# Kernel tuning notes

Measured on AMD Instinct MI355X. Metric: run time of the kernel, lower is better.

The kernel has to match this reference:

```python
import jax, jax.numpy as jnp
import numpy as np

E = 128          # embed_dim
CTX = 3 * E      # context_dim = 384 (graph_emb 2E + node_emb E)
B = 16
N = 1024
D_IN = 2 * CTX   # mamba inner dim (expand=2) = 768
D_ST = 16        # mamba_hidden_dim (SSM state size)
DT_R = CTX // 16 # dt_rank = 24
K = 4            # causal depthwise conv kernel
TAU = 1.0        # gs_tau
ITERS = 5        # gs_iters


def setup_inputs() -> dict:
    key = jax.random.key(0)
    ks = jax.random.split(key, 12)
    s = 0.02
    inp = {
        "graph_emb": jax.random.normal(ks[0], (B, 2 * E), jnp.float32),
        "node_emb": jax.random.normal(ks[1], (B, N, E), jnp.float32),
        "W_key": jax.random.normal(ks[2], (E, CTX), jnp.float32) * s,
        "rms_w": jnp.ones((CTX,), jnp.float32),
        "W_in": jax.random.normal(ks[3], (CTX, 2 * D_IN), jnp.float32) * s,
        "conv_w": jax.random.normal(ks[4], (D_IN, K), jnp.float32) * s,
        "conv_b": jnp.zeros((D_IN,), jnp.float32),
        "W_x": jax.random.normal(ks[5], (D_IN, DT_R + 2 * D_ST), jnp.float32) * s,
        "W_dt": jax.random.normal(ks[6], (DT_R, D_IN), jnp.float32) * s,
        "b_dt": jnp.full((D_IN,), -4.0, jnp.float32),  # softplus -> small positive dt
        "A_log": jnp.log(jnp.tile(jnp.arange(1, D_ST + 1, dtype=jnp.float32), (D_IN, 1))),
        "Dp": jnp.ones((D_IN,), jnp.float32),
        "W_out": jax.random.normal(ks[7], (D_IN, CTX), jnp.float32) * s,
        "gumbel_sink": jax.random.gumbel(ks[8], (B, N, N), jnp.float32),
        "gumbel_sample": jax.random.gumbel(ks[9], (B, N, N), jnp.float32),
    }
    return inp


def _mamba(x, rms_w, W_in, conv_w, conv_b, W_x, W_dt, b_dt, A_log, Dp, W_out):
    # x: (B, N, CTX) -> (B, N, CTX); RMSNorm -> S6 mixer -> residual
    h = x * jax.lax.rsqrt(jnp.mean(x * x, axis=-1, keepdims=True) + 1e-6) * rms_w
    u, z = jnp.split(h @ W_in, 2, axis=-1)              # each (B, N, D_IN)
    # causal depthwise conv over the sequence axis
    uc = jnp.transpose(u, (0, 2, 1))                    # (B, D_IN, N)
    uc = jax.lax.conv_general_dilated(
        uc, conv_w[:, None, :], (1,), [(K - 1, 0)],
        dimension_numbers=("NCH", "OIH", "NCH"), feature_group_count=D_IN)
    u = jax.nn.silu(jnp.transpose(uc, (0, 2, 1)) + conv_b)  # (B, N, D_IN)
    dbc = u @ W_x                                       # (B, N, DT_R + 2*D_ST)
    dt, Bm, Cm = jnp.split(dbc, [DT_R, DT_R + D_ST], axis=-1)
    delta = jax.nn.softplus(dt @ W_dt + b_dt)           # (B, N, D_IN)
    A = -jnp.exp(A_log)                                 # (D_IN, D_ST)

    def step(hst, t):
        u_t, d_t, B_t, C_t = t                          # (B,D_IN),(B,D_IN),(B,D_ST),(B,D_ST)
        dA = jnp.exp(d_t[:, :, None] * A)               # (B, D_IN, D_ST)
        hst = dA * hst + (d_t * u_t)[:, :, None] * B_t[:, None, :]
        y = jnp.sum(hst * C_t[:, None, :], axis=-1)     # (B, D_IN)
        return hst, y

    seq = (jnp.transpose(u, (1, 0, 2)), jnp.transpose(delta, (1, 0, 2)),
           jnp.transpose(Bm, (1, 0, 2)), jnp.transpose(Cm, (1, 0, 2)))
    h0 = jnp.zeros((x.shape[0], D_IN, D_ST), x.dtype)
    _, ys = jax.lax.scan(step, h0, seq)                 # ys: (N, B, D_IN)
    y = jnp.transpose(ys, (1, 0, 2)) + Dp * u
    y = y * jax.nn.silu(z)
    return x + y @ W_out


def reference(graph_emb, node_emb, W_key, rms_w, W_in, conv_w, conv_b, W_x,
              W_dt, b_dt, A_log, Dp, W_out, gumbel_sink, gumbel_sample):
    b, n, _ = node_emb.shape
    keys = node_emb @ W_key                             # (B, N, CTX)
    ctx = jnp.concatenate(
        [jnp.broadcast_to(graph_emb[:, None, :], (b, n, graph_emb.shape[-1])), node_emb], axis=-1)
    queries = _mamba(ctx, rms_w, W_in, conv_w, conv_b, W_x, W_dt, b_dt, A_log, Dp, W_out)
    logits = jnp.einsum("bic,bjc->bij", keys, queries)  # (B, N, N)
    # Gumbel-Sinkhorn in log domain; end on row (axis=2) normalization -> rows are log-probs
    la = (logits + gumbel_sink) / TAU
    for _ in range(ITERS):
        la = la - jax.nn.logsumexp(la, axis=1, keepdims=True)  # column scaling
        la = la - jax.nn.logsumexp(la, axis=2, keepdims=True)  # row scaling
    # sampled tour: per-step categorical via Gumbel-max over rows
    tours = jnp.argmax(la + gumbel_sample, axis=-1)     # (B, N) int
    log_probs = jnp.take_along_axis(la, tours[..., None], axis=2)[..., 0]  # (B, N)
    entropies = -jnp.sum(la * jnp.exp(la), axis=-1)     # (B, N)
    return tours, log_probs, entropies
```

## Files before the change

### kernel.cpp

```cpp
#include <hip/hip_runtime.h>
#include <math.h>

#define Bsz 16
#define Nn  1024
#define Ee  128
#define CTX 384
#define DIN 768
#define DST 16
#define DTR 24
#define ROWS (Bsz*Nn)

__global__ __launch_bounds__(128) void rms_k(
    const float* __restrict__ ge, const float* __restrict__ ne,
    float* __restrict__ rs)
{
    int row = blockIdx.x;
    int b = row >> 10;
    int tid = threadIdx.x;
    float ssq = 0.f;
    #pragma unroll
    for (int k = 0; k < 3; ++k) {
        int idx = tid + k * 128;
        float v = (idx < 256) ? ge[b * 256 + idx]
                              : ne[(long long)row * 128 + (idx - 256)];
        ssq += v * v;
    }
    __shared__ float sh[128];
    sh[tid] = ssq;
    __syncthreads();
    for (int w = 64; w > 0; w >>= 1) {
        if (tid < w) sh[tid] += sh[tid + w];
        __syncthreads();
    }
    if (tid == 0) rs[row] = rsqrtf(sh[0] * (1.f / 384.f) + 1e-6f);
}

__global__ __launch_bounds__(256) void zero_k(float* __restrict__ p, int n)
{
    int i = blockIdx.x * 256 + threadIdx.x;
    if (i < n) p[i] = 0.f;
}

template<int EPI, bool BT, int AMODE>
__global__ __launch_bounds__(256) void gemm_k(
    const float* __restrict__ A, int lda, long long aB,
    const float* __restrict__ Bm, int ldb, long long bB,
    float* __restrict__ C, int ldc, long long cB,
    int M, int N, int K,
    const float* __restrict__ ge, const float* __restrict__ ne,
    const float* __restrict__ rowS, const float* __restrict__ colS,
    const float* __restrict__ bias,
    const float* __restrict__ add, long long addB)
{
    __shared__ float As[16][68];
    __shared__ float Bs[16][68];
    int tid = threadIdx.x;
    int tx = tid & 15, ty = tid >> 4;
    int gn0 = blockIdx.x * 64;
    int rowBase = blockIdx.y * 64;
    int bz = blockIdx.z;
    const float* Ab = A + (long long)bz * aB + (long long)rowBase * lda;
    const float* Bb = Bm + (long long)bz * bB;
    float acc[4][4] = {};

    for (int k0 = 0; k0 < K; k0 += 16) {
        #pragma unroll
        for (int r = 0; r < 4; ++r) {
            int idx = tid + r * 256;
            int m = idx >> 4, kk = idx & 15;
            float v = 0.f;
            if (AMODE == 0) {
                if (k0 + kk < K) v = Ab[(long long)m * lda + k0 + kk];
            } else if (AMODE == 1) {
                int grow = rowBase + m;
                int col = k0 + kk;
                if (col < K) {
                    v = (col < 256) ? ge[(grow >> 10) * 256 + col]
                                    : ne[(long long)grow * 128 + (col - 256)];
                    v *= rowS[grow] * colS[col];
                }
            } else {
                int grow = rowBase + m;
                int col = k0 + kk;
                if (col < K) {
                    v = A[(long long)col * lda + grow];
                    if (AMODE == 3) {
                        float z = rowS[(long long)grow * 768 + col];
                        v *= z / (1.f + __expf(-z));
                    }
                }
            }
            As[kk][m] = v;
        }
        #pragma unroll
        for (int r = 0; r < 4; ++r) {
            int idx = tid + r * 256;
            if (!BT) {
                int n = idx & 63, kk = idx >> 6;
                float v = 0.f;
                if (k0 + kk < K && gn0 + n < N)
                    v = Bb[(long long)(k0 + kk) * ldb + gn0 + n];
                Bs[kk][n] = v;
            } else {
                int kk = idx & 15, n = idx >> 4;
                float v = 0.f;
                if (k0 + kk < K && gn0 + n < N)
                    v = Bb[(long long)(gn0 + n) * ldb + k0 + kk];
                Bs[kk][n] = v;
            }
        }
        __syncthreads();
        #pragma unroll
        for (int kk = 0; kk < 16; ++kk) {
            float4 a4 = *(const float4*)&As[kk][ty * 4];
            float4 b4 = *(const float4*)&Bs[kk][tx * 4];
            float av[4] = {a4.x, a4.y, a4.z, a4.w};
            float bv[4] = {b4.x, b4.y, b4.z, b4.w};
            #pragma unroll
            for (int i = 0; i < 4; ++i)
                #pragma unroll
                for (int j = 0; j < 4; ++j)
                    acc[i][j] = fmaf(av[i], bv[j], acc[i][j]);
        }
        __syncthreads();
    }

    #pragma unroll
    for (int i = 0; i < 4; ++i) {
        int gm = rowBase + ty * 4 + i;
        #pragma unroll
        for (int j = 0; j < 4; ++j) {
            int gn = gn0 + tx * 4 + j;
            if (gn >= N) continue;
            float v = acc[i][j];
            if (EPI == 1) {
                float x = v + bias[gn];
                v = fmaxf(x, 0.f) + log1pf(expf(-fabsf(x)));
            } else if (EPI == 3) {
                v += add[(long long)bz * addB + (long long)gm * (long long)N + gn];
            } else if (EPI == 4) {
                v += (gn < 256) ? ge[(gm >> 10) * 256 + gn]
                                : ne[(long long)gm * 128 + (gn - 256)];
            } else if (EPI == 5) {
                float x = v + bias[gm];
                v = fmaxf(x, 0.f) + log1pf(expf(-fabsf(x)));
            }
            C[(long long)bz * cB + (long long)gm * ldc + gn] = v;
        }
    }
}

__global__ __launch_bounds__(256) void conv_t_k(
    const float* __restrict__ uB, const float* __restrict__ cw,
    const float* __restrict__ cb, float* __restrict__ uT)
{
    __shared__ float tile[67][33];
    int b = blockIdx.z, d0 = blockIdx.y * 32, n0 = blockIdx.x * 64;
    int tid = threadIdx.x;
    for (int i = tid; i < 67 * 32; i += 256) {
        int r = i >> 5, c = i & 31;
        int n = n0 - 3 + r;
        tile[r][c] = (n >= 0) ? uB[((long long)(b * 1024 + n)) * 768 + d0 + c] : 0.f;
    }
    __syncthreads();
    int nl = tid & 63;
    int dh = (tid >> 6) * 8;
    #pragma unroll
    for (int dl = 0; dl < 8; ++dl) {
        int d = dh + dl;
        const float* w = cw + (d0 + d) * 4;
        float acc = cb[d0 + d];
        acc = fmaf(tile[nl][d],     w[0], acc);
        acc = fmaf(tile[nl + 1][d], w[1], acc);
        acc = fmaf(tile[nl + 2][d], w[2], acc);
        acc = fmaf(tile[nl + 3][d], w[3], acc);
        float sv = acc / (1.f + __expf(-acc));
        uT[(long long)(d0 + d) * 16384 + b * 1024 + n0 + nl] = sv;
    }
}

__global__ __launch_bounds__(256) void pack_bc_k(
    const float* __restrict__ dbc, float* __restrict__ TBC)
{
    int c = blockIdx.y;
    int gm = blockIdx.x * 256 + threadIdx.x;
    TBC[(long long)c * 16384 + gm] = dbc[(long long)gm * 56 + 24 + c];
}

__global__ __launch_bounds__(256) void scan2_k(
    const float* __restrict__ dT, float* uyT,
    const float* __restrict__ TBC, const float* __restrict__ A_log,
    const float* __restrict__ Dp)
{
    int tid = threadIdx.x;
    int s = tid & 15, dl = tid >> 4;
    int b = blockIdx.y;
    int d = blockIdx.x * 16 + dl;
    float a = -__expf(A_log[d * 16 + s]);
    float dp = Dp[d];
    long long base = (long long)b * 1024;
    const float* dR = dT + (long long)d * 16384 + base;
    const float* uR = uyT + (long long)d * 16384 + base;
    const float* BR = TBC + (long long)s * 16384 + base;
    const float* CR = TBC + (long long)(16 + s) * 16384 + base;
    float* yR = uyT + (long long)d * 16384 + base;

    float4 dv0 = *(const float4*)(dR);
    float4 dv1 = *(const float4*)(dR + 4);
    float4 uv0 = *(const float4*)(uR);
    float4 uv1 = *(const float4*)(uR + 4);
    float4 Bv0 = *(const float4*)(BR);
    float4 Bv1 = *(const float4*)(BR + 4);
    float4 Cv0 = *(const float4*)(CR);
    float4 Cv1 = *(const float4*)(CR + 4);
    float h = 0.f;

    for (int g = 0; g < 256; ++g) {
        int gp = (g + 2 < 256) ? (g + 2) * 4 : 255 * 4;
        float4 dv2 = *(const float4*)(dR + gp);
        float4 uv2 = *(const float4*)(uR + gp);
        float4 Bv2 = *(const float4*)(BR + gp);
        float4 Cv2 = *(const float4*)(CR + gp);

        float dv[4] = {dv0.x, dv0.y, dv0.z, dv0.w};
        float uv[4] = {uv0.x, uv0.y, uv0.z, uv0.w};
        float Bv[4] = {Bv0.x, Bv0.y, Bv0.z, Bv0.w};
        float Cv[4] = {Cv0.x, Cv0.y, Cv0.z, Cv0.w};
        float ya[4];
        #pragma unroll
        for (int j = 0; j < 4; ++j) {
            float dA = __expf(dv[j] * a);
            h = fmaf(dA, h, dv[j] * uv[j] * Bv[j]);
            float yp = h * Cv[j];
            yp += __shfl_down(yp, 8, 16);
            yp += __shfl_down(yp, 4, 16);
            yp += __shfl_down(yp, 2, 16);
            yp += __shfl_down(yp, 1, 16);
            ya[j] = yp + dp * uv[j];
        }
        if (s == 0) {
            *(float4*)(yR + g * 4) = make_float4(ya[0], ya[1], ya[2], ya[3]);
        }
        dv0 = dv1; dv1 = dv2;
        uv0 = uv1; uv1 = uv2;
        Bv0 = Bv1; Bv1 = Bv2;
        Cv0 = Cv1; Cv1 = Cv2;
    }
}

__global__ __launch_bounds__(256) void col_lse_part(
    const float* __restrict__ la0, const float* __restrict__ R,
    float2* __restrict__ cpart)
{
    int j = blockIdx.x * 256 + threadIdx.x;
    int ch = blockIdx.y;
    int b = blockIdx.z;
    const float* base = la0 + (long long)b * 1024 * 1024 + (long long)ch * 64 * 1024 + j;
    const float* Rb = R + b * 1024 + ch * 64;
    float m = -INFINITY, sum = 0.f;
    for (int i = 0; i < 64; ++i) {
        float x = base[(long long)i * 1024] - Rb[i];
        float nm = fmaxf(m, x);
        sum = sum * expf(m - nm) + expf(x - nm);
        m = nm;
    }
    cpart[(long long)(b * 16 + ch) * 1024 + j] = make_float2(m, sum);
}

__global__ __launch_bounds__(256) void col_comb_k(
    const float2* __restrict__ cpart, float* __restrict__ Cv)
{
    int idx = blockIdx.x * 256 + threadIdx.x;
    int b = idx >> 10, j = idx & 1023;
    float m = -INFINITY, sum = 0.f;
    #pragma unroll
    for (int ch = 0; ch < 16; ++ch) {
        float2 p = cpart[(long long)(b * 16 + ch) * 1024 + j];
        float nm = fmaxf(m, p.x);
        sum = sum * expf(m - nm) + p.y * expf(p.x - nm);
        m = nm;
    }
    Cv[idx] = m + logf(sum);
}

__global__ __launch_bounds__(256) void row_lse_k(
    const float* __restrict__ la0, const float* __restrict__ Cv,
    float* __restrict__ R)
{
    int r = blockIdx.x;
    int b = r >> 10;
    const float* row = la0 + (long long)r * 1024;
    const float* Cb = Cv + b * 1024;
    int tid = threadIdx.x;
    float m = -INFINITY, sum = 0.f;
    #pragma unroll
    for (int k = 0; k < 4; ++k) {
        int j = tid + k * 256;
        float x = row[j] - Cb[j];
        float nm = fmaxf(m, x);
        sum = sum * expf(m - nm) + expf(x - nm);
        m = nm;
    }
    __shared__ float sm[256], ss[256];
    sm[tid] = m; ss[tid] = sum;
    __syncthreads();
    for (int w = 128; w > 0; w >>= 1) {
        if (tid < w) {
            float m2 = sm[tid + w], s2 = ss[tid + w];
            float nm = fmaxf(sm[tid], m2);
            ss[tid] = ss[tid] * expf(sm[tid] - nm) + s2 * expf(m2 - nm);
            sm[tid] = nm;
        }
        __syncthreads();
    }
    if (tid == 0) R[r] = sm[0] + logf(ss[0]);
}

__global__ __launch_bounds__(256) void final_k(
    const float* __restrict__ la0, const float* __restrict__ R,
    const float* __restrict__ Cv, const float* __restrict__ gs,
    float* __restrict__ out)
{
    int r = blockIdx.x;
    int b = r >> 10;
    const float* row = la0 + (long long)r * 1024;
    const float* gr = gs + (long long)r * 1024;
    const float* Cb = Cv + b * 1024;
    float Rvv = R[r];
    int tid = threadIdx.x;
    float bestg = -INFINITY;
    int bestj = 1 << 30;
    float ent = 0.f;
    #pragma unroll
    for (int k = 0; k < 4; ++k) {
        int j = tid + k * 256;
        float la = row[j] - Rvv - Cb[j];
        ent += la * expf(la);
        float g = la + gr[j];
        if (g > bestg || (g == bestg && j < bestj)) { bestg = g; bestj = j; }
    }
    __shared__ float sg[256]; __shared__ int sj[256]; __shared__ float se[256];
    sg[tid] = bestg; sj[tid] = bestj; se[tid] = ent;
    __syncthreads();
    for (int w = 128; w > 0; w >>= 1) {
        if (tid < w) {
            se[tid] += se[tid + w];
            float g2 = sg[tid + w]; int j2 = sj[tid + w];
            if (g2 > sg[tid] || (g2 == sg[tid] && j2 < sj[tid])) {
                sg[tid] = g2; sj[tid] = j2;
            }
        }
        __syncthreads();
    }
    if (tid == 0) {
        int j = sj[0];
        out[r] = (float)j;
        out[16384 + r] = row[j] - Rvv - Cb[j];
        out[32768 + r] = -se[0];
    }
}

extern "C" void kernel_launch(void* const* d_in, const int* in_sizes, int n_in,
                              void* d_out, int out_size, void* d_ws, size_t ws_size,
                              hipStream_t stream)
{
    const float* graph_emb = (const float*)d_in[0];
    const float* node_emb  = (const float*)d_in[1];
    const float* W_key     = (const float*)d_in[2];
    const float* rms_w     = (const float*)d_in[3];
    const float* W_in      = (const float*)d_in[4];
    const float* conv_w    = (const float*)d_in[5];
    const float* conv_b    = (const float*)d_in[6];
    const float* W_x       = (const float*)d_in[7];
    const float* W_dt      = (const float*)d_in[8];
    const float* b_dt      = (const float*)d_in[9];
    const float* A_log     = (const float*)d_in[10];
    const float* Dp        = (const float*)d_in[11];
    const float* W_out     = (const float*)d_in[12];
    const float* g_sink    = (const float*)d_in[13];
    const float* g_samp    = (const float*)d_in[14];
    float* out = (float*)d_out;

    float* ws = (float*)d_ws;
    size_t o = 0;
    auto alloc = [&](size_t nf) { float* p = ws + o; o += nf; return p; };
    float* rs    = alloc(ROWS);
    float* dbc   = alloc((size_t)ROWS * 56);
    float* keys  = alloc((size_t)ROWS * 384);
    float* R1    = alloc((size_t)ROWS * 768);
    float* R2    = alloc((size_t)ROWS * 768);
    float* R3    = alloc((size_t)ROWS * 768);
    float* Rv    = alloc(ROWS);
    float* Cvec  = alloc(ROWS);
    float* cpart = alloc((size_t)16 * 16 * 1024 * 2);
    float* uB      = R1;
    float* deltaT  = R1;
    float* queries = R1;
    float* uT      = R2;
    float* zB      = R3;
    float* la0     = R2;
    float* TBC     = cpart;

    rms_k<<<dim3(ROWS), 128, 0, stream>>>(graph_emb, node_emb, rs);

    gemm_k<0, false, 0><<<dim3(6, 256, 1), 256, 0, stream>>>(
        node_emb, 128, 0, W_key, 384, 0, keys, 384, 0,
        ROWS, 384, 128, nullptr, nullptr, nullptr, nullptr, nullptr, nullptr, 0);

    gemm_k<0, false, 1><<<dim3(12, 256, 1), 256, 0, stream>>>(
        nullptr, 0, 0, W_in, 1536, 0, uB, 768, 0,
        ROWS, 768, 384, graph_emb, node_emb, rs, rms_w, nullptr, nullptr, 0);

    gemm_k<0, false, 1><<<dim3(12, 256, 1), 256, 0, stream>>>(
        nullptr, 0, 0, W_in + 768, 1536, 0, zB, 768, 0,
        ROWS, 768, 384, graph_emb, node_emb, rs, rms_w, nullptr, nullptr, 0);

    conv_t_k<<<dim3(16, 24, 16), 256, 0, stream>>>(uB, conv_w, conv_b, uT);

    gemm_k<0, false, 2><<<dim3(1, 256, 1), 256, 0, stream>>>(
        uT, 16384, 0, W_x, 56, 0, dbc, 56, 0,
        ROWS, 56, 768, nullptr, nullptr, nullptr, nullptr, nullptr, nullptr, 0);

    gemm_k<5, true, 2><<<dim3(256, 12, 1), 256, 0, stream>>>(
        W_dt, 768, 0, dbc, 56, 0, deltaT, 16384, 0,
        768, 16384, 24, nullptr, nullptr, nullptr, nullptr, b_dt, nullptr, 0);

    pack_bc_k<<<dim3(64, 32), 256, 0, stream>>>(dbc, TBC);

    scan2_k<<<dim3(48, 16), 256, 0, stream>>>(deltaT, uT, TBC, A_log, Dp);

    gemm_k<4, false, 3><<<dim3(6, 256, 1), 256, 0, stream>>>(
        uT, 16384, 0, W_out, 384, 0, queries, 384, 0,
        ROWS, 384, 768, graph_emb, node_emb, zB, nullptr, nullptr, nullptr, 0);

    gemm_k<3, true, 0><<<dim3(16, 16, 16), 256, 0, stream>>>(
        keys, 384, (long long)Nn * 384, queries, 384, (long long)Nn * 384,
        la0, 1024, (long long)Nn * Nn,
        1024, 1024, 384, nullptr, nullptr, nullptr, nullptr, nullptr,
        g_sink, (long long)Nn * Nn);

    zero_k<<<dim3(64), 256, 0, stream>>>(Rv, ROWS);
    for (int it = 0; it < 5; ++it) {
        col_lse_part<<<dim3(4, 16, 16), 256, 0, stream>>>(la0, Rv, (float2*)cpart);
        col_comb_k<<<dim3(64), 256, 0, stream>>>((const float2*)cpart, Cvec);
        row_lse_k<<<dim3(ROWS), 256, 0, stream>>>(la0, Cvec, Rv);
    }

    final_k<<<dim3(ROWS), 256, 0, stream>>>(la0, Rv, Cvec, g_samp, out);
}
```

Measured before the change: 1.787 ms.

## Use 128x128 register-blocked GEMM tiles and fuse SiLU gate into scan

Replaces the 64x64 tile / 4x4-per-thread GEMM with a 128x128 tile / 8x8-per-thread version. It uses vectorized float4 global loads and stores, and adds an optional transposed-output path. The z gate is now written transposed so the scan kernel can apply y*silu(z) directly, which removes the transposed gated loads from the out-projection GEMM. The aim is more arithmetic per shared-memory load and cheaper global traffic. The cost is higher register pressure, fewer blocks for the small GEMMs, and a transposed store pattern for z.

```diff
diff --git a/kernel.cpp b/kernel.cpp
--- a/kernel.cpp
+++ b/kernel.cpp
@@ -41,8 +41,8 @@
     if (i < n) p[i] = 0.f;
 }
 
-template<int EPI, bool BT, int AMODE>
-__global__ __launch_bounds__(256) void gemm_k(
+template<int EPI, bool BT, int AMODE, bool CT>
+__global__ __launch_bounds__(256) void gemm2_k(
     const float* __restrict__ A, int lda, long long aB,
     const float* __restrict__ Bm, int ldb, long long bB,
     float* __restrict__ C, int ldc, long long cB,
@@ -52,100 +52,153 @@
     const float* __restrict__ bias,
     const float* __restrict__ add, long long addB)
 {
-    __shared__ float As[16][68];
-    __shared__ float Bs[16][68];
-    int tid = threadIdx.x;
-    int tx = tid & 15, ty = tid >> 4;
-    int gn0 = blockIdx.x * 64;
-    int rowBase = blockIdx.y * 64;
+    __shared__ float As[16][132];
+    __shared__ float Bs[16][132];
+    int t = threadIdx.x;
+    int gn0 = blockIdx.x * 128;
+    int rowBase = blockIdx.y * 128;
     int bz = blockIdx.z;
-    const float* Ab = A + (long long)bz * aB + (long long)rowBase * lda;
+    const float* Abase = A + (long long)bz * aB;
     const float* Bb = Bm + (long long)bz * bB;
-    float acc[4][4] = {};
+    float acc[8][8] = {};
+
+    int cx4 = (t & 15) * 4;
+    int ry4 = (t >> 4) * 4;
 
     for (int k0 = 0; k0 < K; k0 += 16) {
-        #pragma unroll
-        for (int r = 0; r < 4; ++r) {
-            int idx = tid + r * 256;
-            int m = idx >> 4, kk = idx & 15;
-            float v = 0.f;
+        if (AMODE == 0 || AMODE == 1) {
+            int r = t >> 1;
+            int kq = (t & 1) * 8;
+            float av[8];
             if (AMODE == 0) {
-                if (k0 + kk < K) v = Ab[(long long)m * lda + k0 + kk];
-            } else if (AMODE == 1) {
-                int grow = rowBase + m;
-                int col = k0 + kk;
-                if (col < K) {
-                    v = (col < 256) ? ge[(grow >> 10) * 256 + col]
-                                    : ne[(long long)grow * 128 + (col - 256)];
-                    v *= rowS[grow] * colS[col];
-                }
+                const float* Ap = Abase + (long long)(rowBase + r) * lda + k0 + kq;
+                #pragma unroll
+                for (int j = 0; j < 8; ++j)
+                    av[j] = (k0 + kq + j < K) ? Ap[j] : 0.f;
             } else {
-                int grow = rowBase + m;
-                int col = k0 + kk;
-                if (col < K) {
-                    v = A[(long long)col * lda + grow];
-                    if (AMODE == 3) {
-                        float z = rowS[(long long)grow * 768 + col];
-                        v *= z / (1.f + __expf(-z));
+                int grow = rowBase + r;
+                float rsv = rowS[grow];
+                #pragma unroll
+                for (int j = 0; j < 8; ++j) {
+                    int col = k0 + kq + j;
+                    float v = 0.f;
+                    if (col < K) {
+                        v = (col < 256) ? ge[(grow >> 10) * 256 + col]
+                                        : ne[(long long)grow * 128 + (col - 256)];
+                        v *= rsv * colS[col];
                     }
+                    av[j] = v;
                 }
             }
-            As[kk][m] = v;
-        }
-        #pragma unroll
-        for (int r = 0; r < 4; ++r) {
-            int idx = tid + r * 256;
-            if (!BT) {
-                int n = idx & 63, kk = idx >> 6;
-                float v = 0.f;
-                if (k0 + kk < K && gn0 + n < N)
-                    v = Bb[(long long)(k0 + kk) * ldb + gn0 + n];
-                Bs[kk][n] = v;
-            } else {
-                int kk = idx & 15, n = idx >> 4;
-                float v = 0.f;
-                if (k0 + kk < K && gn0 + n < N)
-                    v = Bb[(long long)(gn0 + n) * ldb + k0 + kk];
-                Bs[kk][n] = v;
+            #pragma unroll
+            for (int j = 0; j < 8; ++j) As[kq + j][r] = av[j];
+        } else {
+            int kk = t >> 4;
+            int m0 = (t & 15) * 8;
+            const float* Ap = Abase + (long long)(k0 + kk) * lda + rowBase + m0;
+            float4 v0 = make_float4(0.f, 0.f, 0.f, 0.f), v1 = v0;
+            if (k0 + kk < K) {
+                v0 = *(const float4*)Ap;
+                v1 = *(const float4*)(Ap + 4);
             }
+            *(float4*)&As[kk][m0] = v0;
+            *(float4*)&As[kk][m0 + 4] = v1;
+        }
+        if (!BT) {
+            int kk = t >> 4;
+            int n0 = (t & 15) * 8;
+            const float* Bp = Bb + (long long)(k0 + kk) * ldb + gn0 + n0;
+            float4 v0 = make_float4(0.f, 0.f, 0.f, 0.f), v1 = v0;
+            if (k0 + kk < K) {
+                if (gn0 + n0 + 7 < N) {
+                    v0 = *(const float4*)Bp;
+                    v1 = *(const float4*)(Bp + 4);
+                } else {
+                    float tmp[8];
+                    #pragma unroll
+                    for (int j = 0; j < 8; ++j)
+                        tmp[j] = (gn0 + n0 + j < N) ? Bp[j] : 0.f;
+                    v0 = make_float4(tmp[0], tmp[1], tmp[2], tmp[3]);
+                    v1 = make_float4(tmp[4], tmp[5], tmp[6], tmp[7]);
+                }
+            }
+            *(float4*)&Bs[kk][n0] = v0;
+            *(float4*)&Bs[kk][n0 + 4] = v1;
+        } else {
+            int n = t >> 1;
+            int kq = (t & 1) * 8;
+            const float* Bp = Bb + (long long)(gn0 + n) * ldb + k0 + kq;
+            float bv[8];
+            bool nok = (gn0 + n < N);
+            #pragma unroll
+            for (int j = 0; j < 8; ++j)
+                bv[j] = (nok && k0 + kq + j < K) ? Bp[j] : 0.f;
+            #pragma unroll
+            for (int j = 0; j < 8; ++j) Bs[kq + j][n] = bv[j];
         }
         __syncthreads();
         #pragma unroll
         for (int kk = 0; kk < 16; ++kk) {
-            float4 a4 = *(const float4*)&As[kk][ty * 4];
-            float4 b4 = *(const float4*)&Bs[kk][tx * 4];
-            float av[4] = {a4.x, a4.y, a4.z, a4.w};
-            float bv[4] = {b4.x, b4.y, b4.z, b4.w};
+            float4 a0 = *(const float4*)&As[kk][ry4];
+            float4 a1 = *(const float4*)&As[kk][ry4 + 64];
+            float4 b0 = *(const float4*)&Bs[kk][cx4];
+            float4 b1 = *(const float4*)&Bs[kk][cx4 + 64];
+            float av[8] = {a0.x, a0.y, a0.z, a0.w, a1.x, a1.y, a1.z, a1.w};
+            float bv[8] = {b0.x, b0.y, b0.z, b0.w, b1.x, b1.y, b1.z, b1.w};
             #pragma unroll
-            for (int i = 0; i < 4; ++i)
+            for (int i = 0; i < 8; ++i)
                 #pragma unroll
-                for (int j = 0; j < 4; ++j)
+                for (int j = 0; j < 8; ++j)
                     acc[i][j] = fmaf(av[i], bv[j], acc[i][j]);
         }
         __syncthreads();
     }
 
-    #pragma unroll
-    for (int i = 0; i < 4; ++i) {
-        int gm = rowBase + ty * 4 + i;
+    if (CT) {
         #pragma unroll
-        for (int j = 0; j < 4; ++j) {
-            int gn = gn0 + tx * 4 + j;
-            if (gn >= N) continue;
-            float v = acc[i][j];
-            if (EPI == 1) {
-                float x = v + bias[gn];
-                v = fmaxf(x, 0.f) + log1pf(expf(-fabsf(x)));
-            } else if (EPI == 3) {
-                v += add[(long long)bz * addB + (long long)gm * (long long)N + gn];
-            } else if (EPI == 4) {
-                v += (gn < 256) ? ge[(gm >> 10) * 256 + gn]
-                                : ne[(long long)gm * 128 + (gn - 256)];
-            } else if (EPI == 5) {
-                float x = v + bias[gm];
-                v = fmaxf(x, 0.f) + log1pf(expf(-fabsf(x)));
+        for (int j = 0; j < 8; ++j) {
+            int gn = gn0 + (j >> 2) * 64 + cx4 + (j & 3);
+            #pragma unroll
+            for (int ih = 0; ih < 2; ++ih) {
+                int gmb = rowBase + ih * 64 + ry4;
+                float4 v = make_float4(acc[ih * 4 + 0][j], acc[ih * 4 + 1][j],
+                                       acc[ih * 4 + 2][j], acc[ih * 4 + 3][j]);
+                *(float4*)&C[(long long)gn * ldc + gmb] = v;
             }
-            C[(long long)bz * cB + (long long)gm * ldc + gn] = v;
+        }
+    } else {
+        float* Cb = C + (long long)bz * cB;
+        #pragma unroll
+        for (int i = 0; i < 8; ++i) {
+            int gm = rowBase + (i >> 2) * 64 + ry4 + (i & 3);
+            #pragma unroll
+            for (int jh = 0; jh < 2; ++jh) {
+                int gn = gn0 + jh * 64 + cx4;
+                float v[4];
+                #pragma unroll
+                for (int e = 0; e < 4; ++e) {
+                    float x = acc[i][jh * 4 + e];
+                    if (EPI == 3) {
+                        x += add[(long long)bz * addB + (long long)gm * (long long)N + gn + e];
+                    } else if (EPI == 4) {
+                        int c = gn + e;
+                        x += (c < 256) ? ge[(gm >> 10) * 256 + c]
+                                       : ne[(long long)gm * 128 + (c - 256)];
+                    } else if (EPI == 5) {
+                        float s = x + bias[gm];
+                        x = fmaxf(s, 0.f) + log1pf(expf(-fabsf(s)));
+                    }
+                    v[e] = x;
+                }
+                if (gn + 3 < N) {
+                    *(float4*)&Cb[(long long)gm * ldc + gn] =
+                        make_float4(v[0], v[1], v[2], v[3]);
+                } else {
+                    #pragma unroll
+                    for (int e = 0; e < 4; ++e)
+                        if (gn + e < N) Cb[(long long)gm * ldc + gn + e] = v[e];
+                }
+            }
         }
     }
 }
@@ -187,8 +240,8 @@
     TBC[(long long)c * 16384 + gm] = dbc[(long long)gm * 56 + 24 + c];
 }
 
-__global__ __launch_bounds__(256) void scan2_k(
-    const float* __restrict__ dT, float* uyT,
+__global__ __launch_bounds__(256) void scan3_k(
+    const float* __restrict__ dT, float* uyT, const float* __restrict__ zT,
     const float* __restrict__ TBC, const float* __restrict__ A_log,
     const float* __restrict__ Dp)
 {
@@ -201,6 +254,7 @@
     long long base = (long long)b * 1024;
     const float* dR = dT + (long long)d * 16384 + base;
     const float* uR = uyT + (long long)d * 16384 + base;
+    const float* zR = zT + (long long)d * 16384 + base;
     const float* BR = TBC + (long long)s * 16384 + base;
     const float* CR = TBC + (long long)(16 + s) * 16384 + base;
     float* yR = uyT + (long long)d * 16384 + base;
@@ -209,6 +263,8 @@
     float4 dv1 = *(const float4*)(dR + 4);
     float4 uv0 = *(const float4*)(uR);
     float4 uv1 = *(const float4*)(uR + 4);
+    float4 zv0 = *(const float4*)(zR);
+    float4 zv1 = *(const float4*)(zR + 4);
     float4 Bv0 = *(const float4*)(BR);
     float4 Bv1 = *(const float4*)(BR + 4);
     float4 Cv0 = *(const float4*)(CR);
@@ -219,11 +275,13 @@
         int gp = (g + 2 < 256) ? (g + 2) * 4 : 255 * 4;
         float4 dv2 = *(const float4*)(dR + gp);
         float4 uv2 = *(const float4*)(uR + gp);
+        float4 zv2 = *(const float4*)(zR + gp);
         float4 Bv2 = *(const float4*)(BR + gp);
         float4 Cv2 = *(const float4*)(CR + gp);
 
         float dv[4] = {dv0.x, dv0.y, dv0.z, dv0.w};
         float uv[4] = {uv0.x, uv0.y, uv0.z, uv0.w};
+        float zv[4] = {zv0.x, zv0.y, zv0.z, zv0.w};
         float Bv[4] = {Bv0.x, Bv0.y, Bv0.z, Bv0.w};
         float Cv[4] = {Cv0.x, Cv0.y, Cv0.z, Cv0.w};
         float ya[4];
@@ -236,13 +294,15 @@
             yp += __shfl_down(yp, 4, 16);
             yp += __shfl_down(yp, 2, 16);
             yp += __shfl_down(yp, 1, 16);
-            ya[j] = yp + dp * uv[j];
+            float z = zv[j];
+            ya[j] = (yp + dp * uv[j]) * (z / (1.f + __expf(-z)));
         }
         if (s == 0) {
             *(float4*)(yR + g * 4) = make_float4(ya[0], ya[1], ya[2], ya[3]);
         }
         dv0 = dv1; dv1 = dv2;
         uv0 = uv1; uv1 = uv2;
+        zv0 = zv1; zv1 = zv2;
         Bv0 = Bv1; Bv1 = Bv2;
         Cv0 = Cv1; Cv1 = Cv2;
     }
@@ -397,43 +457,43 @@
     float* deltaT  = R1;
     float* queries = R1;
     float* uT      = R2;
-    float* zB      = R3;
+    float* zT      = R3;
     float* la0     = R2;
     float* TBC     = cpart;
 
     rms_k<<<dim3(ROWS), 128, 0, stream>>>(graph_emb, node_emb, rs);
 
-    gemm_k<0, false, 0><<<dim3(6, 256, 1), 256, 0, stream>>>(
+    gemm2_k<0, false, 0, false><<<dim3(3, 128, 1), 256, 0, stream>>>(
         node_emb, 128, 0, W_key, 384, 0, keys, 384, 0,
         ROWS, 384, 128, nullptr, nullptr, nullptr, nullptr, nullptr, nullptr, 0);
 
-    gemm_k<0, false, 1><<<dim3(12, 256, 1), 256, 0, stream>>>(
+    gemm2_k<0, false, 1, false><<<dim3(6, 128, 1), 256, 0, stream>>>(
         nullptr, 0, 0, W_in, 1536, 0, uB, 768, 0,
         ROWS, 768, 384, graph_emb, node_emb, rs, rms_w, nullptr, nullptr, 0);
 
-    gemm_k<0, false, 1><<<dim3(12, 256, 1), 256, 0, stream>>>(
-        nullptr, 0, 0, W_in + 768, 1536, 0, zB, 768, 0,
+    gemm2_k<0, false, 1, true><<<dim3(6, 128, 1), 256, 0, stream>>>(
+        nullptr, 0, 0, W_in + 768, 1536, 0, zT, 16384, 0,
         ROWS, 768, 384, graph_emb, node_emb, rs, rms_w, nullptr, nullptr, 0);
 
     conv_t_k<<<dim3(16, 24, 16), 256, 0, stream>>>(uB, conv_w, conv_b, uT);
 
-    gemm_k<0, false, 2><<<dim3(1, 256, 1), 256, 0, stream>>>(
+    gemm2_k<0, false, 2, false><<<dim3(1, 128, 1), 256, 0, stream>>>(
         uT, 16384, 0, W_x, 56, 0, dbc, 56, 0,
         ROWS, 56, 768, nullptr, nullptr, nullptr, nullptr, nullptr, nullptr, 0);
 
-    gemm_k<5, true, 2><<<dim3(256, 12, 1), 256, 0, stream>>>(
+    gemm2_k<5, true, 2, false><<<dim3(128, 6, 1), 256, 0, stream>>>(
         W_dt, 768, 0, dbc, 56, 0, deltaT, 16384, 0,
         768, 16384, 24, nullptr, nullptr, nullptr, nullptr, b_dt, nullptr, 0);
 
     pack_bc_k<<<dim3(64, 32), 256, 0, stream>>>(dbc, TBC);
 
-    scan2_k<<<dim3(48, 16), 256, 0, stream>>>(deltaT, uT, TBC, A_log, Dp);
-
-    gemm_k<4, false, 3><<<dim3(6, 256, 1), 256, 0, stream>>>(
+    scan3_k<<<dim3(48, 16), 256, 0, stream>>>(deltaT, uT, zT, TBC, A_log, Dp);
+
+    gemm2_k<4, false, 2, false><<<dim3(3, 128, 1), 256, 0, stream>>>(
         uT, 16384, 0, W_out, 384, 0, queries, 384, 0,
-        ROWS, 384, 768, graph_emb, node_emb, zB, nullptr, nullptr, nullptr, 0);
-
-    gemm_k<3, true, 0><<<dim3(16, 16, 16), 256, 0, stream>>>(
+        ROWS, 384, 768, graph_emb, node_emb, nullptr, nullptr, nullptr, nullptr, 0);
+
+    gemm2_k<3, true, 0, false><<<dim3(8, 8, 16), 256, 0, stream>>>(
         keys, 384, (long long)Nn * 384, queries, 384, (long long)Nn * 384,
         la0, 1024, (long long)Nn * Nn,
         1024, 1024, 384, nullptr, nullptr, nullptr, nullptr, nullptr,
```

New measurement: 1.604 ms. 1.11x faster.
